# Kernel tuning notes

Hardware: AMD Instinct MI355X
Metric: run time of the kernel (lower is better)

Reference implementation:

```python
import jax, jax.numpy as jnp
import numpy as np

EPS = 1e-5  # BatchNorm eps


def _conv(x, w, pad):
    # NCHW / OIHW stride-1 convolution (matches nn.Conv2d(..., padding=pad, bias=False))
    return jax.lax.conv_general_dilated(
        x, w, window_strides=(1, 1), padding=[(pad, pad), (pad, pad)],
        dimension_numbers=("NCHW", "OIHW", "NCHW"))


def _bn2d(x, g, b, m, v):
    # inference-mode BN folded to a per-channel affine
    s = g * jax.lax.rsqrt(v + EPS)
    return x * s[None, :, None, None] + (b - m * s)[None, :, None, None]


def _pool2(x):
    # AvgPool2d(2): non-overlapping 2x2 mean
    n, c, h, w = x.shape
    return x.reshape(n, c, h // 2, 2, w // 2, 2).mean(axis=(3, 5))


def _block(x, w, g, b, m, v):
    # Conv -> BN -> ReLU -> AvgPool2 -> Hardtanh(0,1)
    x = _conv(x, w, pad=2)
    x = _bn2d(x, g, b, m, v)
    x = jax.nn.relu(x)
    x = _pool2(x)
    return jnp.clip(x, 0.0, 1.0)


def setup_inputs() -> dict:
    key = jax.random.key(0)
    ks = jax.random.split(key, 24)
    B = 1024
    x = jax.random.uniform(ks[0], (B, 3, 32, 32), dtype=jnp.float32)

    def wgt(k, shape):
        fan_in = shape[1] * shape[2] * shape[3]
        return jax.random.normal(k, shape, jnp.float32) / np.float32(np.sqrt(fan_in))

    def bn(k, c):
        k1, k2, k3, k4 = jax.random.split(k, 4)
        g = jax.random.uniform(k1, (c,), jnp.float32, 0.5, 1.5)
        b = jax.random.normal(k2, (c,), jnp.float32) * 0.1
        m = jax.random.normal(k3, (c,), jnp.float32) * 0.1
        v = jax.random.uniform(k4, (c,), jnp.float32, 0.5, 1.5)
        return g, b, m, v

    w1 = wgt(ks[1], (32, 3, 5, 5))
    w2 = wgt(ks[2], (32, 32, 5, 5))
    w3 = wgt(ks[3], (64, 32, 5, 5))
    w4 = wgt(ks[4], (10, 64, 4, 4))  # fc1 as a 4x4 valid conv
    g1, b1, m1, v1 = bn(ks[5], 32)
    g2, b2, m2, v2 = bn(ks[6], 32)
    g3, b3, m3, v3 = bn(ks[7], 64)
    g4, b4, m4, v4 = bn(ks[8], 10)
    return dict(x=x,
                w1=w1, g1=g1, b1=b1, m1=m1, v1=v1,
                w2=w2, g2=g2, b2=b2, m2=m2, v2=v2,
                w3=w3, g3=g3, b3=b3, m3=m3, v3=v3,
                w4=w4, g4=g4, b4=b4, m4=m4, v4=v4)


def reference(x,
              w1, g1, b1, m1, v1,
              w2, g2, b2, m2, v2,
              w3, g3, b3, m3, v3,
              w4, g4, b4, m4, v4):
    x = _block(x, w1, g1, b1, m1, v1)   # [B,32,16,16]
    x = _block(x, w2, g2, b2, m2, v2)   # [B,32,8,8]
    x = _block(x, w3, g3, b3, m3, v3)   # [B,64,4,4]
    x = _conv(x, w4, pad=0)             # [B,10,1,1]
    x = x.reshape(x.shape[0], -1)       # flatten -> [B,10]
    s = g4 * jax.lax.rsqrt(v4 + EPS)    # BatchNorm1d_fixed (inference affine)
    return x * s[None, :] + (b4 - m4 * s)[None, :]
```

## Files before the change

### kernel.cpp

```cpp
#include <hip/hip_runtime.h>
#include <hip/hip_bf16.h>

#define EPS 1e-5f

typedef __bf16 v8bf __attribute__((ext_vector_type(8)));
typedef __bf16 v4bf __attribute__((ext_vector_type(4)));
typedef float  v4f  __attribute__((ext_vector_type(4)));

__global__ void k_wtrans(const float* __restrict__ w1, const float* __restrict__ w2,
                         const float* __restrict__ w3,
                         __hip_bfloat16* __restrict__ fb1, __hip_bfloat16* __restrict__ fb2,
                         __hip_bfloat16* __restrict__ fb3)
{
    int idx = blockIdx.x * 256 + threadIdx.x;
    if (idx < 640) {
        int lane = idx & 63, fi = idx >> 6;
        int ky = fi >> 1, nt = fi & 1;
        int oc = nt * 16 + (lane & 15), k0 = (lane >> 4) * 8;
        __hip_bfloat16* dst = fb1 + idx * 8;
        #pragma unroll
        for (int j = 0; j < 8; ++j) {
            int k = k0 + j, dx = k >> 2, ic = k & 3;
            float val = (dx < 5 && ic < 3) ? w1[oc * 75 + ic * 25 + ky * 5 + dx] : 0.f;
            dst[j] = __float2bfloat16(val);
        }
    } else if (idx < 640 + 3200) {
        int k2 = idx - 640;
        int lane = k2 & 63, fi = k2 >> 6;
        int tap = fi >> 1, nt = fi & 1;
        int oc = nt * 16 + (lane & 15), ic0 = (lane >> 4) * 8;
        __hip_bfloat16* dst = fb2 + k2 * 8;
        #pragma unroll
        for (int j = 0; j < 8; ++j)
            dst[j] = __float2bfloat16(w2[oc * 800 + (ic0 + j) * 25 + tap]);
    } else if (idx < 640 + 3200 + 6400) {
        int k3 = idx - 3840;
        int lane = k3 & 63, fi = k3 >> 6;
        int tap = fi >> 2, nt = fi & 3;
        int oc = nt * 16 + (lane & 15), ic0 = (lane >> 4) * 8;
        __hip_bfloat16* dst = fb3 + k3 * 8;
        #pragma unroll
        for (int j = 0; j < 8; ++j)
            dst[j] = __float2bfloat16(w3[oc * 800 + (ic0 + j) * 25 + tap]);
    }
}

__global__ __launch_bounds__(512, 4) void k_fused(
    const float* __restrict__ x,
    const __hip_bfloat16* __restrict__ fb1,
    const __hip_bfloat16* __restrict__ fb2,
    const __hip_bfloat16* __restrict__ fb3,
    const float* __restrict__ w4,
    const float* __restrict__ g1, const float* __restrict__ b1,
    const float* __restrict__ m1, const float* __restrict__ v1,
    const float* __restrict__ g2, const float* __restrict__ b2,
    const float* __restrict__ m2, const float* __restrict__ v2,
    const float* __restrict__ g3, const float* __restrict__ b3,
    const float* __restrict__ m3, const float* __restrict__ v3,
    const float* __restrict__ g4, const float* __restrict__ b4,
    const float* __restrict__ m4, const float* __restrict__ v4,
    float* __restrict__ out)
{
    __shared__ __align__(16) unsigned char pool[43840];
    __shared__ float sc1[32], bi1[32], sc2[32], bi2[32], sc3[64], bi3[64];

    __hip_bfloat16 (*xs2)[20][40] = (__hip_bfloat16(*)[20][40])pool;
    __hip_bfloat16 (*xs1)[40][4]  = (__hip_bfloat16(*)[40][4])(pool + 32000);
    __hip_bfloat16 (*xs3)[12][40] = (__hip_bfloat16(*)[12][40])(pool + 32000);
    float* fin = (float*)pool;

    const int img = blockIdx.x, t = threadIdx.x;
    const int lane = t & 63, wave = t >> 6;
    const int lo = lane & 15, hi = lane >> 4;

    const int nt1 = wave & 1;
    v8bf bw[5];
    #pragma unroll
    for (int ky = 0; ky < 5; ++ky)
        bw[ky] = *(const v8bf*)(fb1 + ((ky * 2 + nt1) * 64 + lane) * 8);

    for (int i = t; i < 2740; i += 512) ((uint4*)pool)[i] = make_uint4(0, 0, 0, 0);
    if (t < 32) {
        float s = g1[t] * rsqrtf(v1[t] + EPS); sc1[t] = s; bi1[t] = b1[t] - m1[t] * s;
        float u = g2[t] * rsqrtf(v2[t] + EPS); sc2[t] = u; bi2[t] = b2[t] - m2[t] * u;
    }
    if (t < 64) {
        float s = g3[t] * rsqrtf(v3[t] + EPS); sc3[t] = s; bi3[t] = b3[t] - m3[t] * s;
    }
    __syncthreads();

    for (int i = t; i < 768; i += 512) {
        float4 val = *(const float4*)(x + (size_t)img * 3072 + i * 4);
        int ic = i >> 8, rem = i & 255;
        int y = rem >> 3, xx = (rem & 7) * 4;
        xs1[y + 2][xx + 2][ic] = __float2bfloat16(val.x);
        xs1[y + 2][xx + 3][ic] = __float2bfloat16(val.y);
        xs1[y + 2][xx + 4][ic] = __float2bfloat16(val.z);
        xs1[y + 2][xx + 5][ic] = __float2bfloat16(val.w);
    }
    __syncthreads();

    {
        const int prg = wave >> 1;
        #pragma unroll
        for (int pi = 0; pi < 4; ++pi) {
            const int pr = prg + pi * 4;
            const int y0 = 2 * pr;
            v4f acc[2][2];
            #pragma unroll
            for (int a0 = 0; a0 < 2; ++a0)
                #pragma unroll
                for (int a1 = 0; a1 < 2; ++a1)
                    acc[a0][a1] = (v4f){0.f, 0.f, 0.f, 0.f};

            #pragma unroll
            for (int xh = 0; xh < 2; ++xh) {
                const int xx = xh * 16 + lo + hi * 2;
                v8bf av[6];
                #pragma unroll
                for (int r = 0; r < 6; ++r) {
                    v4bf lo4 = *(const v4bf*)&xs1[y0 + r][xx][0];
                    v4bf hi4 = *(const v4bf*)&xs1[y0 + r][xx + 1][0];
                    av[r] = __builtin_shufflevector(lo4, hi4, 0, 1, 2, 3, 4, 5, 6, 7);
                }
                #pragma unroll
                for (int ky = 0; ky < 5; ++ky) {
                    acc[0][xh] = __builtin_amdgcn_mfma_f32_16x16x32_bf16(av[ky],     bw[ky], acc[0][xh], 0, 0, 0);
                    acc[1][xh] = __builtin_amdgcn_mfma_f32_16x16x32_bf16(av[ky + 1], bw[ky], acc[1][xh], 0, 0, 0);
                }
            }
            const int oc = nt1 * 16 + lo;
            const float s = sc1[oc], bb = bi1[oc];
            #pragma unroll
            for (int xh = 0; xh < 2; ++xh) {
                float u0 = fmaxf(fmaf(acc[0][xh][0], s, bb), 0.f);
                float u1 = fmaxf(fmaf(acc[0][xh][1], s, bb), 0.f);
                float u2 = fmaxf(fmaf(acc[0][xh][2], s, bb), 0.f);
                float u3 = fmaxf(fmaf(acc[0][xh][3], s, bb), 0.f);
                float q0 = fmaxf(fmaf(acc[1][xh][0], s, bb), 0.f);
                float q1 = fmaxf(fmaf(acc[1][xh][1], s, bb), 0.f);
                float q2 = fmaxf(fmaf(acc[1][xh][2], s, bb), 0.f);
                float q3 = fmaxf(fmaf(acc[1][xh][3], s, bb), 0.f);
                float p0 = fminf(0.25f * (u0 + u1 + q0 + q1), 1.f);
                float p1 = fminf(0.25f * (u2 + u3 + q2 + q3), 1.f);
                const int px = xh * 8 + hi * 2;
                xs2[pr + 2][px + 2][oc] = __float2bfloat16(p0);
                xs2[pr + 2][px + 3][oc] = __float2bfloat16(p1);
            }
        }
    }
    __syncthreads();

    {
        uint4* p3 = (uint4*)(pool + 32000);
        for (int i = t; i < 720; i += 512) p3[i] = make_uint4(0, 0, 0, 0);
    }
    __syncthreads();

    {
        const int nt = wave & 1, wgrp = wave >> 1;
        v4f acc[2][2];
        #pragma unroll
        for (int a0 = 0; a0 < 2; ++a0)
            #pragma unroll
            for (int a1 = 0; a1 < 2; ++a1)
                acc[a0][a1] = (v4f){0.f, 0.f, 0.f, 0.f};

        v8bf bf[5];
        #pragma unroll
        for (int ky = 0; ky < 5; ++ky)
            bf[ky] = *(const v8bf*)(fb2 + ((ky * 5 + 0) * 2 + nt) * 512 + lane * 8);

        #pragma unroll
        for (int kx = 0; kx < 5; ++kx) {
            v8bf bfn[5];
            if (kx < 4) {
                #pragma unroll
                for (int ky = 0; ky < 5; ++ky)
                    bfn[ky] = *(const v8bf*)(fb2 + ((ky * 5 + kx + 1) * 2 + nt) * 512 + lane * 8);
            }
            v8bf av[8];
            #pragma unroll
            for (int r = 0; r < 8; ++r)
                av[r] = *(const v8bf*)&xs2[wgrp * 4 + r][lo + kx][hi * 8];
            #pragma unroll
            for (int ky = 0; ky < 5; ++ky) {
                acc[0][0] = __builtin_amdgcn_mfma_f32_16x16x32_bf16(av[ky],     bf[ky], acc[0][0], 0, 0, 0);
                acc[0][1] = __builtin_amdgcn_mfma_f32_16x16x32_bf16(av[ky + 1], bf[ky], acc[0][1], 0, 0, 0);
                acc[1][0] = __builtin_amdgcn_mfma_f32_16x16x32_bf16(av[ky + 2], bf[ky], acc[1][0], 0, 0, 0);
                acc[1][1] = __builtin_amdgcn_mfma_f32_16x16x32_bf16(av[ky + 3], bf[ky], acc[1][1], 0, 0, 0);
            }
            if (kx < 4) {
                #pragma unroll
                for (int ky = 0; ky < 5; ++ky) bf[ky] = bfn[ky];
            }
        }

        const int oc = nt * 16 + lo;
        const float s = sc2[oc], bb = bi2[oc];
        #pragma unroll
        for (int rpi = 0; rpi < 2; ++rpi) {
            const int rp = wgrp * 2 + rpi;
            float u0 = fmaxf(fmaf(acc[rpi][0][0], s, bb), 0.f);
            float u1 = fmaxf(fmaf(acc[rpi][0][1], s, bb), 0.f);
            float u2 = fmaxf(fmaf(acc[rpi][0][2], s, bb), 0.f);
            float u3 = fmaxf(fmaf(acc[rpi][0][3], s, bb), 0.f);
            float q0 = fmaxf(fmaf(acc[rpi][1][0], s, bb), 0.f);
            float q1 = fmaxf(fmaf(acc[rpi][1][1], s, bb), 0.f);
            float q2 = fmaxf(fmaf(acc[rpi][1][2], s, bb), 0.f);
            float q3 = fmaxf(fmaf(acc[rpi][1][3], s, bb), 0.f);
            float p0 = fminf(0.25f * (u0 + u1 + q0 + q1), 1.f);
            float p1 = fminf(0.25f * (u2 + u3 + q2 + q3), 1.f);
            xs3[rp + 2][hi * 2 + 2][oc] = __float2bfloat16(p0);
            xs3[rp + 2][hi * 2 + 3][oc] = __float2bfloat16(p1);
        }
    }
    __syncthreads();

    {
        const int nt = wave >> 1, mh = wave & 1;
        const int oc = nt * 16 + lo;
        const int ya0 = lo >> 3, xa = lo & 7;
        v4f acc[2];
        #pragma unroll
        for (int q = 0; q < 2; ++q) acc[q] = (v4f){0.f, 0.f, 0.f, 0.f};

        v8bf bf[5];
        #pragma unroll
        for (int kx = 0; kx < 5; ++kx)
            bf[kx] = *(const v8bf*)(fb3 + ((0 * 5 + kx) * 4 + nt) * 512 + lane * 8);

        #pragma unroll
        for (int ky = 0; ky < 5; ++ky) {
            v8bf bfn[5];
            if (ky < 4) {
                #pragma unroll
                for (int kx = 0; kx < 5; ++kx)
                    bfn[kx] = *(const v8bf*)(fb3 + (((ky + 1) * 5 + kx) * 4 + nt) * 512 + lane * 8);
            }
            #pragma unroll
            for (int kx = 0; kx < 5; ++kx) {
                #pragma unroll
                for (int mi = 0; mi < 2; ++mi) {
                    const int mt = mh * 2 + mi;
                    v8bf av = *(const v8bf*)&xs3[2 * mt + ya0 + ky][xa + kx][hi * 8];
                    acc[mi] = __builtin_amdgcn_mfma_f32_16x16x32_bf16(av, bf[kx], acc[mi], 0, 0, 0);
                }
            }
            if (ky < 4) {
                #pragma unroll
                for (int kx = 0; kx < 5; ++kx) bf[kx] = bfn[kx];
            }
        }

        const float s = sc3[oc], bb = bi3[oc];
        const int xb = (hi & 1) * 2;
        #pragma unroll
        for (int mi = 0; mi < 2; ++mi) {
            const int mt = mh * 2 + mi;
            float v0 = fmaxf(fmaf(acc[mi][0], s, bb), 0.f);
            float v1 = fmaxf(fmaf(acc[mi][1], s, bb), 0.f);
            float v2 = fmaxf(fmaf(acc[mi][2], s, bb), 0.f);
            float v3 = fmaxf(fmaf(acc[mi][3], s, bb), 0.f);
            float s01 = v0 + v1, s23 = v2 + v3;
            float o01 = __shfl_xor(s01, 32);
            float o23 = __shfl_xor(s23, 32);
            float p0 = fminf(0.25f * (s01 + o01), 1.f);
            float p1 = fminf(0.25f * (s23 + o23), 1.f);
            if (hi < 2) {
                fin[oc * 16 + mt * 4 + xb]     = p0;
                fin[oc * 16 + mt * 4 + xb + 1] = p1;
            }
        }
    }
    __syncthreads();

    {
        for (int oc = wave; oc < 10; oc += 8) {
            const float4* wp = (const float4*)(w4 + oc * 1024);
            const float4* fp = (const float4*)fin;
            float acc0 = 0.f, acc1 = 0.f;
            #pragma unroll
            for (int ch = 0; ch < 4; ++ch) {
                float4 a = fp[ch * 64 + lane];
                float4 w = wp[ch * 64 + lane];
                acc0 = fmaf(a.x, w.x, acc0); acc1 = fmaf(a.y, w.y, acc1);
                acc0 = fmaf(a.z, w.z, acc0); acc1 = fmaf(a.w, w.w, acc1);
            }
            float acc = acc0 + acc1;
            acc += __shfl_xor(acc, 1);
            acc += __shfl_xor(acc, 2);
            acc += __shfl_xor(acc, 4);
            acc += __shfl_xor(acc, 8);
            acc += __shfl_xor(acc, 16);
            acc += __shfl_xor(acc, 32);
            if (lane == 0) {
                float s = g4[oc] * rsqrtf(v4[oc] + EPS);
                out[img * 10 + oc] = acc * s + (b4[oc] - m4[oc] * s);
            }
        }
    }
}

extern "C" void kernel_launch(void* const* d_in, const int* in_sizes, int n_in,
                              void* d_out, int out_size, void* d_ws, size_t ws_size,
                              hipStream_t stream) {
    const float* x  = (const float*)d_in[0];
    const float* w1 = (const float*)d_in[1];
    const float* g1 = (const float*)d_in[2];
    const float* b1 = (const float*)d_in[3];
    const float* m1 = (const float*)d_in[4];
    const float* v1 = (const float*)d_in[5];
    const float* w2 = (const float*)d_in[6];
    const float* g2 = (const float*)d_in[7];
    const float* b2 = (const float*)d_in[8];
    const float* m2 = (const float*)d_in[9];
    const float* v2 = (const float*)d_in[10];
    const float* w3 = (const float*)d_in[11];
    const float* g3 = (const float*)d_in[12];
    const float* b3 = (const float*)d_in[13];
    const float* m3 = (const float*)d_in[14];
    const float* v3 = (const float*)d_in[15];
    const float* w4 = (const float*)d_in[16];
    const float* g4 = (const float*)d_in[17];
    const float* b4 = (const float*)d_in[18];
    const float* m4 = (const float*)d_in[19];
    const float* v4 = (const float*)d_in[20];
    float* out = (float*)d_out;

    char* base = (char*)d_ws;
    __hip_bfloat16* fb1 = (__hip_bfloat16*)base;
    __hip_bfloat16* fb2 = (__hip_bfloat16*)(base + 16384);
    __hip_bfloat16* fb3 = (__hip_bfloat16*)(base + 67584);

    k_wtrans<<<40, 256, 0, stream>>>(w1, w2, w3, fb1, fb2, fb3);
    k_fused<<<1024, 512, 0, stream>>>(x, fb1, fb2, fb3, w4,
                                      g1, b1, m1, v1, g2, b2, m2, v2,
                                      g3, b3, m3, v3, g4, b4, m4, v4, out);
}
```

Baseline: 39.93 us.

## Swizzle LDS activation layouts, shrink shared memory, restructure conv1 wave mapping

Replaces the padded [.][.][40] activation buffers with unpadded 32-channel rows whose 8-channel blocks are XOR-swizzled by column, and packs the input tile tighter. Together these cut LDS from about 43.8KB to 36.8KB, and launch bounds are raised to request 8 blocks per CU. Conv1 is reorganised so each wave handles 4 input rows for both output-channel tiles, reusing the loaded A fragments across 8 MFMAs. The separate zeroing pass and barrier for the conv3 input halo are merged into the conv2 phase, clearing only the border region. In exchange, register pressure rises under the tighter launch bound, and the swizzle address maths adds ALU work.

Measured after the change: 96.93 us. +142.7%, slower.

```diff
diff --git a/kernel.cpp b/kernel.cpp
--- a/kernel.cpp
+++ b/kernel.cpp
@@ -45,7 +45,13 @@
     }
 }
 
-__global__ __launch_bounds__(512, 4) void k_fused(
+#define XS2(row, col, blk) ((__hip_bfloat16*)(pool + (((((row)*20 + (col))*32) + (((blk) ^ ((col)&3))*8))*2)))
+#define XS2S(row, col, oc) ((__hip_bfloat16*)(pool + (((((row)*20 + (col))*32) + ((((oc)>>3) ^ ((col)&3))*8) + ((oc)&7))*2)))
+#define XS1(row, col)      ((__hip_bfloat16*)(pool + 25600 + ((((row)*39 + (col))*4)*2)))
+#define XS3(row, col, blk) ((__hip_bfloat16*)(pool + 25600 + (((((row)*12 + (col))*32) + (((blk) ^ ((col)&3))*8))*2)))
+#define XS3S(row, col, oc) ((__hip_bfloat16*)(pool + 25600 + (((((row)*12 + (col))*32) + ((((oc)>>3) ^ ((col)&3))*8) + ((oc)&7))*2)))
+
+__global__ __launch_bounds__(512, 8) void k_fused(
     const float* __restrict__ x,
     const __hip_bfloat16* __restrict__ fb1,
     const __hip_bfloat16* __restrict__ fb2,
@@ -61,25 +67,22 @@
     const float* __restrict__ m4, const float* __restrict__ v4,
     float* __restrict__ out)
 {
-    __shared__ __align__(16) unsigned char pool[43840];
+    __shared__ __align__(16) unsigned char pool[36832];
     __shared__ float sc1[32], bi1[32], sc2[32], bi2[32], sc3[64], bi3[64];
-
-    __hip_bfloat16 (*xs2)[20][40] = (__hip_bfloat16(*)[20][40])pool;
-    __hip_bfloat16 (*xs1)[40][4]  = (__hip_bfloat16(*)[40][4])(pool + 32000);
-    __hip_bfloat16 (*xs3)[12][40] = (__hip_bfloat16(*)[12][40])(pool + 32000);
     float* fin = (float*)pool;
 
     const int img = blockIdx.x, t = threadIdx.x;
     const int lane = t & 63, wave = t >> 6;
     const int lo = lane & 15, hi = lane >> 4;
 
-    const int nt1 = wave & 1;
-    v8bf bw[5];
+    v8bf bw[5][2];
     #pragma unroll
     for (int ky = 0; ky < 5; ++ky)
-        bw[ky] = *(const v8bf*)(fb1 + ((ky * 2 + nt1) * 64 + lane) * 8);
-
-    for (int i = t; i < 2740; i += 512) ((uint4*)pool)[i] = make_uint4(0, 0, 0, 0);
+        #pragma unroll
+        for (int nt = 0; nt < 2; ++nt)
+            bw[ky][nt] = *(const v8bf*)(fb1 + ((ky * 2 + nt) * 64 + lane) * 8);
+
+    for (int i = t; i < 2302; i += 512) ((uint4*)pool)[i] = make_uint4(0, 0, 0, 0);
     if (t < 32) {
         float s = g1[t] * rsqrtf(v1[t] + EPS); sc1[t] = s; bi1[t] = b1[t] - m1[t] * s;
         float u = g2[t] * rsqrtf(v2[t] + EPS); sc2[t] = u; bi2[t] = b2[t] - m2[t] * u;
@@ -93,71 +96,81 @@
         float4 val = *(const float4*)(x + (size_t)img * 3072 + i * 4);
         int ic = i >> 8, rem = i & 255;
         int y = rem >> 3, xx = (rem & 7) * 4;
-        xs1[y + 2][xx + 2][ic] = __float2bfloat16(val.x);
-        xs1[y + 2][xx + 3][ic] = __float2bfloat16(val.y);
-        xs1[y + 2][xx + 4][ic] = __float2bfloat16(val.z);
-        xs1[y + 2][xx + 5][ic] = __float2bfloat16(val.w);
+        XS1(y + 2, xx + 2)[ic] = __float2bfloat16(val.x);
+        XS1(y + 2, xx + 3)[ic] = __float2bfloat16(val.y);
+        XS1(y + 2, xx + 4)[ic] = __float2bfloat16(val.z);
+        XS1(y + 2, xx + 5)[ic] = __float2bfloat16(val.w);
     }
     __syncthreads();
 
     {
-        const int prg = wave >> 1;
-        #pragma unroll
-        for (int pi = 0; pi < 4; ++pi) {
-            const int pr = prg + pi * 4;
-            const int y0 = 2 * pr;
-            v4f acc[2][2];
+        const int y0 = 4 * wave;
+        #pragma unroll
+        for (int xh = 0; xh < 2; ++xh) {
+            const int xx = xh * 16 + lo + hi * 2;
+            v8bf av[8];
+            #pragma unroll
+            for (int r = 0; r < 8; ++r) {
+                v4bf lo4 = *(const v4bf*)XS1(y0 + r, xx);
+                v4bf hi4 = *(const v4bf*)XS1(y0 + r, xx + 1);
+                av[r] = __builtin_shufflevector(lo4, hi4, 0, 1, 2, 3, 4, 5, 6, 7);
+            }
+            v4f acc[2][2][2];
             #pragma unroll
             for (int a0 = 0; a0 < 2; ++a0)
                 #pragma unroll
                 for (int a1 = 0; a1 < 2; ++a1)
-                    acc[a0][a1] = (v4f){0.f, 0.f, 0.f, 0.f};
-
-            #pragma unroll
-            for (int xh = 0; xh < 2; ++xh) {
-                const int xx = xh * 16 + lo + hi * 2;
-                v8bf av[6];
-                #pragma unroll
-                for (int r = 0; r < 6; ++r) {
-                    v4bf lo4 = *(const v4bf*)&xs1[y0 + r][xx][0];
-                    v4bf hi4 = *(const v4bf*)&xs1[y0 + r][xx + 1][0];
-                    av[r] = __builtin_shufflevector(lo4, hi4, 0, 1, 2, 3, 4, 5, 6, 7);
+                    #pragma unroll
+                    for (int a2 = 0; a2 < 2; ++a2)
+                        acc[a0][a1][a2] = (v4f){0.f, 0.f, 0.f, 0.f};
+            #pragma unroll
+            for (int ky = 0; ky < 5; ++ky)
+                #pragma unroll
+                for (int nt = 0; nt < 2; ++nt) {
+                    acc[0][0][nt] = __builtin_amdgcn_mfma_f32_16x16x32_bf16(av[ky],     bw[ky][nt], acc[0][0][nt], 0, 0, 0);
+                    acc[0][1][nt] = __builtin_amdgcn_mfma_f32_16x16x32_bf16(av[ky + 1], bw[ky][nt], acc[0][1][nt], 0, 0, 0);
+                    acc[1][0][nt] = __builtin_amdgcn_mfma_f32_16x16x32_bf16(av[ky + 2], bw[ky][nt], acc[1][0][nt], 0, 0, 0);
+                    acc[1][1][nt] = __builtin_amdgcn_mfma_f32_16x16x32_bf16(av[ky + 3], bw[ky][nt], acc[1][1][nt], 0, 0, 0);
                 }
-                #pragma unroll
-                for (int ky = 0; ky < 5; ++ky) {
-                    acc[0][xh] = __builtin_amdgcn_mfma_f32_16x16x32_bf16(av[ky],     bw[ky], acc[0][xh], 0, 0, 0);
-                    acc[1][xh] = __builtin_amdgcn_mfma_f32_16x16x32_bf16(av[ky + 1], bw[ky], acc[1][xh], 0, 0, 0);
+            #pragma unroll
+            for (int pri = 0; pri < 2; ++pri)
+                #pragma unroll
+                for (int nt = 0; nt < 2; ++nt) {
+                    const int oc = nt * 16 + lo;
+                    const float s = sc1[oc], bb = bi1[oc];
+                    float u0 = fmaxf(fmaf(acc[pri][0][nt][0], s, bb), 0.f);
+                    float u1 = fmaxf(fmaf(acc[pri][0][nt][1], s, bb), 0.f);
+                    float u2 = fmaxf(fmaf(acc[pri][0][nt][2], s, bb), 0.f);
+                    float u3 = fmaxf(fmaf(acc[pri][0][nt][3], s, bb), 0.f);
+                    float q0 = fmaxf(fmaf(acc[pri][1][nt][0], s, bb), 0.f);
+                    float q1 = fmaxf(fmaf(acc[pri][1][nt][1], s, bb), 0.f);
+                    float q2 = fmaxf(fmaf(acc[pri][1][nt][2], s, bb), 0.f);
+                    float q3 = fmaxf(fmaf(acc[pri][1][nt][3], s, bb), 0.f);
+                    float p0 = fminf(0.25f * (u0 + u1 + q0 + q1), 1.f);
+                    float p1 = fminf(0.25f * (u2 + u3 + q2 + q3), 1.f);
+                    const int pr = 2 * wave + pri;
+                    const int px = xh * 8 + hi * 2;
+                    *XS2S(pr + 2, px + 2, oc) = __float2bfloat16(p0);
+                    *XS2S(pr + 2, px + 3, oc) = __float2bfloat16(p1);
                 }
-            }
-            const int oc = nt1 * 16 + lo;
-            const float s = sc1[oc], bb = bi1[oc];
-            #pragma unroll
-            for (int xh = 0; xh < 2; ++xh) {
-                float u0 = fmaxf(fmaf(acc[0][xh][0], s, bb), 0.f);
-                float u1 = fmaxf(fmaf(acc[0][xh][1], s, bb), 0.f);
-                float u2 = fmaxf(fmaf(acc[0][xh][2], s, bb), 0.f);
-                float u3 = fmaxf(fmaf(acc[0][xh][3], s, bb), 0.f);
-                float q0 = fmaxf(fmaf(acc[1][xh][0], s, bb), 0.f);
-                float q1 = fmaxf(fmaf(acc[1][xh][1], s, bb), 0.f);
-                float q2 = fmaxf(fmaf(acc[1][xh][2], s, bb), 0.f);
-                float q3 = fmaxf(fmaf(acc[1][xh][3], s, bb), 0.f);
-                float p0 = fminf(0.25f * (u0 + u1 + q0 + q1), 1.f);
-                float p1 = fminf(0.25f * (u2 + u3 + q2 + q3), 1.f);
-                const int px = xh * 8 + hi * 2;
-                xs2[pr + 2][px + 2][oc] = __float2bfloat16(p0);
-                xs2[pr + 2][px + 3][oc] = __float2bfloat16(p1);
-            }
         }
     }
     __syncthreads();
 
     {
-        uint4* p3 = (uint4*)(pool + 32000);
-        for (int i = t; i < 720; i += 512) p3[i] = make_uint4(0, 0, 0, 0);
-    }
-    __syncthreads();
-
-    {
+        uint* x3u = (uint*)(pool + 25600);
+        for (int i = t; i < 1280; i += 512) {
+            int u;
+            if (i < 384)      u = i;
+            else if (i < 768) u = 1920 + (i - 384);
+            else {
+                int j = i - 768;
+                int r = 2 + (j >> 6), c = j & 63;
+                u = r * 192 + (c < 32 ? c : 128 + c);
+            }
+            x3u[u] = 0u;
+        }
+
         const int nt = wave & 1, wgrp = wave >> 1;
         v4f acc[2][2];
         #pragma unroll
@@ -182,7 +195,7 @@
             v8bf av[8];
             #pragma unroll
             for (int r = 0; r < 8; ++r)
-                av[r] = *(const v8bf*)&xs2[wgrp * 4 + r][lo + kx][hi * 8];
+                av[r] = *(const v8bf*)XS2(4 * wgrp + r, lo + kx, hi);
             #pragma unroll
             for (int ky = 0; ky < 5; ++ky) {
                 acc[0][0] = __builtin_amdgcn_mfma_f32_16x16x32_bf16(av[ky],     bf[ky], acc[0][0], 0, 0, 0);
@@ -199,20 +212,20 @@
         const int oc = nt * 16 + lo;
         const float s = sc2[oc], bb = bi2[oc];
         #pragma unroll
-        for (int rpi = 0; rpi < 2; ++rpi) {
-            const int rp = wgrp * 2 + rpi;
-            float u0 = fmaxf(fmaf(acc[rpi][0][0], s, bb), 0.f);
-            float u1 = fmaxf(fmaf(acc[rpi][0][1], s, bb), 0.f);
-            float u2 = fmaxf(fmaf(acc[rpi][0][2], s, bb), 0.f);
-            float u3 = fmaxf(fmaf(acc[rpi][0][3], s, bb), 0.f);
-            float q0 = fmaxf(fmaf(acc[rpi][1][0], s, bb), 0.f);
-            float q1 = fmaxf(fmaf(acc[rpi][1][1], s, bb), 0.f);
-            float q2 = fmaxf(fmaf(acc[rpi][1][2], s, bb), 0.f);
-            float q3 = fmaxf(fmaf(acc[rpi][1][3], s, bb), 0.f);
+        for (int pri = 0; pri < 2; ++pri) {
+            const int rp = wgrp * 2 + pri;
+            float u0 = fmaxf(fmaf(acc[pri][0][0], s, bb), 0.f);
+            float u1 = fmaxf(fmaf(acc[pri][0][1], s, bb), 0.f);
+            float u2 = fmaxf(fmaf(acc[pri][0][2], s, bb), 0.f);
+            float u3 = fmaxf(fmaf(acc[pri][0][3], s, bb), 0.f);
+            float q0 = fmaxf(fmaf(acc[pri][1][0], s, bb), 0.f);
+            float q1 = fmaxf(fmaf(acc[pri][1][1], s, bb), 0.f);
+            float q2 = fmaxf(fmaf(acc[pri][1][2], s, bb), 0.f);
+            float q3 = fmaxf(fmaf(acc[pri][1][3], s, bb), 0.f);
             float p0 = fminf(0.25f * (u0 + u1 + q0 + q1), 1.f);
             float p1 = fminf(0.25f * (u2 + u3 + q2 + q3), 1.f);
-            xs3[rp + 2][hi * 2 + 2][oc] = __float2bfloat16(p0);
-            xs3[rp + 2][hi * 2 + 3][oc] = __float2bfloat16(p1);
+            *XS3S(rp + 2, hi * 2 + 2, oc) = __float2bfloat16(p0);
+            *XS3S(rp + 2, hi * 2 + 3, oc) = __float2bfloat16(p1);
         }
     }
     __syncthreads();
@@ -243,7 +256,7 @@
                 #pragma unroll
                 for (int mi = 0; mi < 2; ++mi) {
                     const int mt = mh * 2 + mi;
-                    v8bf av = *(const v8bf*)&xs3[2 * mt + ya0 + ky][xa + kx][hi * 8];
+                    v8bf av = *(const v8bf*)XS3(2 * mt + ya0 + ky, xa + kx, hi);
                     acc[mi] = __builtin_amdgcn_mfma_f32_16x16x32_bf16(av, bf[kx], acc[mi], 0, 0, 0);
                 }
             }
```
